# Kernel optimization log

Hardware: AMD Instinct MI355X
Metric: run time of the kernel (lower is better)

The kernel has to match this reference:

```python
import jax, jax.numpy as jnp
import numpy as np

NUM_CLASSES = 10
TAU = 3.3333333


def thermometer_encode(x, thresholds):
    # x: [B, F], thresholds: [F, T] -> binary bits [B, F*T]
    bits = (x[:, :, None] > thresholds[None, :, :]).astype(x.dtype)
    B = x.shape[0]
    return bits.reshape(B, -1)


def lut_layer(h, idx, luts):
    # h: [B, I] activations in [0,1]; idx: [O, n] input mapping; luts: [O, 2^n]
    # Multilinear interpolation over the 2^n LUT corners (gather + fold).
    xs = h[:, idx]                       # [B, O, n] gathered inputs
    B, O, n = xs.shape
    acc = jnp.broadcast_to(luts[None, :, :], (B, O, luts.shape[1]))  # [B, O, 2^n]
    for k in range(n):                   # fold one input bit per step (MSB first)
        half = acc.shape[-1] // 2
        xk = xs[:, :, k:k + 1]           # [B, O, 1]
        acc = acc[..., :half] * (1.0 - xk) + acc[..., half:] * xk
    return acc[..., 0]                   # [B, O]


def group_sum(h, k, tau):
    # h: [B, W] -> [B, k] popcount-style grouped sum scaled by 1/tau
    B, W = h.shape
    return h.reshape(B, k, W // k).sum(axis=-1) / tau


def setup_inputs() -> dict:
    key = jax.random.key(0)
    ks = jax.random.split(key, 6)
    B, F, T = 512, 1024, 3
    I = F * T                            # 3072 thermometer bits
    O1, O2, n = 2000, 1000, 6
    x = jax.random.normal(ks[0], (B, F), dtype=jnp.float32)
    thresholds = jax.random.normal(ks[1], (F, T), dtype=jnp.float32)
    luts1 = jax.random.uniform(ks[2], (O1, 2 ** n), dtype=jnp.float32)
    idx1 = jax.random.randint(ks[3], (O1, n), 0, I, dtype=jnp.int32)
    luts2 = jax.random.uniform(ks[4], (O2, 2 ** n), dtype=jnp.float32)
    idx2 = jax.random.randint(ks[5], (O2, n), 0, O1, dtype=jnp.int32)
    return {"x": x, "thresholds": thresholds, "luts1": luts1, "idx1": idx1,
            "luts2": luts2, "idx2": idx2}


def reference(x, thresholds, luts1, idx1, luts2, idx2):
    h = thermometer_encode(x, thresholds)     # [B, 3072] binary
    h = lut_layer(h, idx1, luts1)             # [B, 2000]
    h = lut_layer(h, idx2, luts2)             # [B, 1000]
    return group_sum(h, NUM_CLASSES, TAU)     # [B, 10]
```

## Files before the change

### kernel.cpp

```cpp
#include <hip/hip_runtime.h>


#define BATCH 512
#define FEAT  1024
#define NBITS (FEAT * 3)
#define O1    2000
#define O2    1000
#define NCLS  10
#define G     2
#define NT    512

__global__ __launch_bounds__(NT) void dwn_fused2(
    const float* __restrict__ x,
    const float* __restrict__ thr,
    const float* __restrict__ luts1,
    const int*   __restrict__ idx1,
    const float* __restrict__ luts2,
    const int*   __restrict__ idx2,
    float* __restrict__ out)
{
    __shared__ unsigned char s_bits[G][NBITS];
    __shared__ float s_h1[G][O1];
    __shared__ float s_h2[G][O2];
    __shared__ float s_part[G * NCLS * 10];

    const int b0 = blockIdx.x * G;
    const int t  = threadIdx.x;

    for (int i = t; i < G * FEAT; i += NT) {
        int r = i >> 10;
        int f = i & (FEAT - 1);
        float xv = x[(b0 + r) * FEAT + f];
        const float* tp = thr + f * 3;
        s_bits[r][f * 3 + 0] = (unsigned char)(xv > tp[0]);
        s_bits[r][f * 3 + 1] = (unsigned char)(xv > tp[1]);
        s_bits[r][f * 3 + 2] = (unsigned char)(xv > tp[2]);
    }
    __syncthreads();

    for (int i = t; i < G * O1; i += NT) {
        int o = i >> 1;
        int r = i & 1;
        const int2* ip = (const int2*)(idx1 + o * 6);
        int2 p0 = ip[0], p1 = ip[1], p2 = ip[2];
        int code = ((int)s_bits[r][p0.x] << 5) | ((int)s_bits[r][p0.y] << 4)
                 | ((int)s_bits[r][p1.x] << 3) | ((int)s_bits[r][p1.y] << 2)
                 | ((int)s_bits[r][p2.x] << 1) |  (int)s_bits[r][p2.y];
        s_h1[r][o] = luts1[o * 64 + code];
    }
    __syncthreads();

    for (int i = t; i < G * O2; i += NT) {
        int o = i >> 1;
        int r = i & 1;
        const int2* ip = (const int2*)(idx2 + o * 6);
        int2 p0 = ip[0], p1 = ip[1], p2 = ip[2];
        float xv0 = s_h1[r][p0.x];
        float xv1 = s_h1[r][p0.y];
        float xv2 = s_h1[r][p1.x];
        float xv3 = s_h1[r][p1.y];
        float xv4 = s_h1[r][p2.x];
        float xv5 = s_h1[r][p2.y];

        const float4* lp = (const float4*)(luts2 + (size_t)o * 64);
        float v[16];
#pragma unroll
        for (int q = 0; q < 16; ++q) {
            float4 e = lp[q];
            float u0 = e.x + xv5 * (e.y - e.x);
            float u1 = e.z + xv5 * (e.w - e.z);
            v[q] = u0 + xv4 * (u1 - u0);
        }
#pragma unroll
        for (int q = 0; q < 8; ++q) v[q] = v[2*q] + xv3 * (v[2*q+1] - v[2*q]);
#pragma unroll
        for (int q = 0; q < 4; ++q) v[q] = v[2*q] + xv2 * (v[2*q+1] - v[2*q]);
#pragma unroll
        for (int q = 0; q < 2; ++q) v[q] = v[2*q] + xv1 * (v[2*q+1] - v[2*q]);
        s_h2[r][o] = v[0] + xv0 * (v[1] - v[0]);
    }
    __syncthreads();

    if (t < G * NCLS * 10) {
        int g = t / 10;
        int p = t % 10;
        int r   = g / NCLS;
        int cls = g % NCLS;
        const float* hp = &s_h2[r][cls * 100 + p * 10];
        float s = 0.0f;
#pragma unroll
        for (int j = 0; j < 10; ++j) s += hp[j];
        s_part[t] = s;
    }
    __syncthreads();
    if (t < G * NCLS) {
        float s = 0.0f;
#pragma unroll
        for (int j = 0; j < 10; ++j) s += s_part[t * 10 + j];
        int r   = t / NCLS;
        int cls = t % NCLS;
        out[(b0 + r) * NCLS + cls] = s / 3.3333333f;
    }
}

extern "C" void kernel_launch(void* const* d_in, const int* in_sizes, int n_in,
                              void* d_out, int out_size, void* d_ws, size_t ws_size,
                              hipStream_t stream) {
    const float* x      = (const float*)d_in[0];
    const float* thr    = (const float*)d_in[1];
    const float* luts1  = (const float*)d_in[2];
    const int*   idx1   = (const int*)  d_in[3];
    const float* luts2  = (const float*)d_in[4];
    const int*   idx2   = (const int*)  d_in[5];
    float* out = (float*)d_out;

    dwn_fused2<<<BATCH / G, NT, 0, stream>>>(x, thr, luts1, idx1, luts2, idx2, out);
}
```

Measured before the change: 79.32 us.

## Split fused kernel into four batch-transposed kernels with ballot-packed bitmasks

Replaces the single fused kernel, which ran 256 blocks of 2 batch rows each, with four kernels. They pack the thermometer bits into wave-ballot 64-bit masks, compute layer 1 and layer 2 with one block per output neuron and one thread per batch row, then reduce the classes. Intermediates live transposed in workspace memory so accesses along the batch are coalesced, and each block's LUT row and index entry are shared by all threads. The cost is global-memory round trips for h1/h2 (about 4 MB plus 2 MB) and three extra kernel launches in exchange for far more parallelism.

Result: slower. 82.33 us (+3.8%).

```diff
diff --git a/kernel.cpp b/kernel.cpp
--- a/kernel.cpp
+++ b/kernel.cpp
@@ -1,118 +1,141 @@
 #include <hip/hip_runtime.h>
 
 
-#define BATCH 512
 #define FEAT  1024
-#define NBITS (FEAT * 3)
 #define O1    2000
 #define O2    1000
 #define NCLS  10
-#define G     2
-#define NT    512
 
-__global__ __launch_bounds__(NT) void dwn_fused2(
+#define WS_BITS_OFF  0
+#define WS_H1_OFF    (256 << 10)
+#define WS_H2_OFF    ((256 << 10) + (4 << 20))
+
+__global__ __launch_bounds__(512) void k1_thermo_pack(
     const float* __restrict__ x,
     const float* __restrict__ thr,
+    unsigned long long* __restrict__ bitsT)
+{
+    const int r    = threadIdx.x;
+    const int w    = r >> 6;
+    const int lane = r & 63;
+    const int f0   = blockIdx.x * 4;
+
+    float4 xv4 = *(const float4*)(x + (size_t)r * FEAT + f0);
+    float xa[4] = {xv4.x, xv4.y, xv4.z, xv4.w};
+
+#pragma unroll
+    for (int f = 0; f < 4; ++f) {
+        const float* tp = thr + (size_t)(f0 + f) * 3;
+#pragma unroll
+        for (int j = 0; j < 3; ++j) {
+            unsigned long long m = __ballot(xa[f] > tp[j]);
+            if (lane == 0)
+                bitsT[(size_t)((f0 + f) * 3 + j) * 8 + w] = m;
+        }
+    }
+}
+
+__global__ __launch_bounds__(512) void k2_layer1(
+    const int*   __restrict__ idx1,
     const float* __restrict__ luts1,
-    const int*   __restrict__ idx1,
+    const unsigned long long* __restrict__ bitsT,
+    float* __restrict__ h1T)
+{
+    const int o    = blockIdx.x;
+    const int r    = threadIdx.x;
+    const int w    = r >> 6;
+    const int lane = r & 63;
+    const int* ip  = idx1 + o * 6;
+
+    unsigned long long m0 = bitsT[(size_t)ip[0] * 8 + w];
+    unsigned long long m1 = bitsT[(size_t)ip[1] * 8 + w];
+    unsigned long long m2 = bitsT[(size_t)ip[2] * 8 + w];
+    unsigned long long m3 = bitsT[(size_t)ip[3] * 8 + w];
+    unsigned long long m4 = bitsT[(size_t)ip[4] * 8 + w];
+    unsigned long long m5 = bitsT[(size_t)ip[5] * 8 + w];
+
+    int code = ((int)((m0 >> lane) & 1ull) << 5)
+             | ((int)((m1 >> lane) & 1ull) << 4)
+             | ((int)((m2 >> lane) & 1ull) << 3)
+             | ((int)((m3 >> lane) & 1ull) << 2)
+             | ((int)((m4 >> lane) & 1ull) << 1)
+             |  (int)((m5 >> lane) & 1ull);
+
+    h1T[(size_t)o * 512 + r] = luts1[o * 64 + code];
+}
+
+__global__ __launch_bounds__(512) void k3_layer2(
+    const int*   __restrict__ idx2,
     const float* __restrict__ luts2,
-    const int*   __restrict__ idx2,
+    const float* __restrict__ h1T,
+    float* __restrict__ h2T)
+{
+    const int o   = blockIdx.x;
+    const int r   = threadIdx.x;
+    const int* ip = idx2 + o * 6;
+
+    float xv0 = h1T[(size_t)ip[0] * 512 + r];
+    float xv1 = h1T[(size_t)ip[1] * 512 + r];
+    float xv2 = h1T[(size_t)ip[2] * 512 + r];
+    float xv3 = h1T[(size_t)ip[3] * 512 + r];
+    float xv4 = h1T[(size_t)ip[4] * 512 + r];
+    float xv5 = h1T[(size_t)ip[5] * 512 + r];
+
+    const float4* lp = (const float4*)(luts2 + (size_t)o * 64);
+    float v[16];
+#pragma unroll
+    for (int q = 0; q < 16; ++q) {
+        float4 e = lp[q];
+        float u0 = e.x + xv5 * (e.y - e.x);
+        float u1 = e.z + xv5 * (e.w - e.z);
+        v[q] = u0 + xv4 * (u1 - u0);
+    }
+#pragma unroll
+    for (int q = 0; q < 8; ++q) v[q] = v[2*q] + xv3 * (v[2*q+1] - v[2*q]);
+#pragma unroll
+    for (int q = 0; q < 4; ++q) v[q] = v[2*q] + xv2 * (v[2*q+1] - v[2*q]);
+#pragma unroll
+    for (int q = 0; q < 2; ++q) v[q] = v[2*q] + xv1 * (v[2*q+1] - v[2*q]);
+    h2T[(size_t)o * 512 + r] = v[0] + xv0 * (v[1] - v[0]);
+}
+
+__global__ __launch_bounds__(256) void k4_reduce(
+    const float* __restrict__ h2T,
     float* __restrict__ out)
 {
-    __shared__ unsigned char s_bits[G][NBITS];
-    __shared__ float s_h1[G][O1];
-    __shared__ float s_h2[G][O2];
-    __shared__ float s_part[G * NCLS * 10];
+    const int c = blockIdx.x >> 1;
+    const int r = ((blockIdx.x & 1) << 8) | threadIdx.x;
+    const float* hp = h2T + (size_t)c * 100 * 512 + r;
 
-    const int b0 = blockIdx.x * G;
-    const int t  = threadIdx.x;
-
-    for (int i = t; i < G * FEAT; i += NT) {
-        int r = i >> 10;
-        int f = i & (FEAT - 1);
-        float xv = x[(b0 + r) * FEAT + f];
-        const float* tp = thr + f * 3;
-        s_bits[r][f * 3 + 0] = (unsigned char)(xv > tp[0]);
-        s_bits[r][f * 3 + 1] = (unsigned char)(xv > tp[1]);
-        s_bits[r][f * 3 + 2] = (unsigned char)(xv > tp[2]);
+    float s = 0.0f;
+#pragma unroll
+    for (int p = 0; p < 10; ++p) {
+        float s2 = 0.0f;
+#pragma unroll
+        for (int j = 0; j < 10; ++j) s2 += hp[(size_t)(p * 10 + j) * 512];
+        s += s2;
     }
-    __syncthreads();
-
-    for (int i = t; i < G * O1; i += NT) {
-        int o = i >> 1;
-        int r = i & 1;
-        const int2* ip = (const int2*)(idx1 + o * 6);
-        int2 p0 = ip[0], p1 = ip[1], p2 = ip[2];
-        int code = ((int)s_bits[r][p0.x] << 5) | ((int)s_bits[r][p0.y] << 4)
-                 | ((int)s_bits[r][p1.x] << 3) | ((int)s_bits[r][p1.y] << 2)
-                 | ((int)s_bits[r][p2.x] << 1) |  (int)s_bits[r][p2.y];
-        s_h1[r][o] = luts1[o * 64 + code];
-    }
-    __syncthreads();
-
-    for (int i = t; i < G * O2; i += NT) {
-        int o = i >> 1;
-        int r = i & 1;
-        const int2* ip = (const int2*)(idx2 + o * 6);
-        int2 p0 = ip[0], p1 = ip[1], p2 = ip[2];
-        float xv0 = s_h1[r][p0.x];
-        float xv1 = s_h1[r][p0.y];
-        float xv2 = s_h1[r][p1.x];
-        float xv3 = s_h1[r][p1.y];
-        float xv4 = s_h1[r][p2.x];
-        float xv5 = s_h1[r][p2.y];
-
-        const float4* lp = (const float4*)(luts2 + (size_t)o * 64);
-        float v[16];
-#pragma unroll
-        for (int q = 0; q < 16; ++q) {
-            float4 e = lp[q];
-            float u0 = e.x + xv5 * (e.y - e.x);
-            float u1 = e.z + xv5 * (e.w - e.z);
-            v[q] = u0 + xv4 * (u1 - u0);
-        }
-#pragma unroll
-        for (int q = 0; q < 8; ++q) v[q] = v[2*q] + xv3 * (v[2*q+1] - v[2*q]);
-#pragma unroll
-        for (int q = 0; q < 4; ++q) v[q] = v[2*q] + xv2 * (v[2*q+1] - v[2*q]);
-#pragma unroll
-        for (int q = 0; q < 2; ++q) v[q] = v[2*q] + xv1 * (v[2*q+1] - v[2*q]);
-        s_h2[r][o] = v[0] + xv0 * (v[1] - v[0]);
-    }
-    __syncthreads();
-
-    if (t < G * NCLS * 10) {
-        int g = t / 10;
-        int p = t % 10;
-        int r   = g / NCLS;
-        int cls = g % NCLS;
-        const float* hp = &s_h2[r][cls * 100 + p * 10];
-        float s = 0.0f;
-#pragma unroll
-        for (int j = 0; j < 10; ++j) s += hp[j];
-        s_part[t] = s;
-    }
-    __syncthreads();
-    if (t < G * NCLS) {
-        float s = 0.0f;
-#pragma unroll
-        for (int j = 0; j < 10; ++j) s += s_part[t * 10 + j];
-        int r   = t / NCLS;
-        int cls = t % NCLS;
-        out[(b0 + r) * NCLS + cls] = s / 3.3333333f;
-    }
+    out[r * NCLS + c] = s / 3.3333333f;
 }
 
 extern "C" void kernel_launch(void* const* d_in, const int* in_sizes, int n_in,
                               void* d_out, int out_size, void* d_ws, size_t ws_size,
                               hipStream_t stream) {
-    const float* x      = (const float*)d_in[0];
-    const float* thr    = (const float*)d_in[1];
-    const float* luts1  = (const float*)d_in[2];
-    const int*   idx1   = (const int*)  d_in[3];
-    const float* luts2  = (const float*)d_in[4];
-    const int*   idx2   = (const int*)  d_in[5];
+    const float* x     = (const float*)d_in[0];
+    const float* thr   = (const float*)d_in[1];
+    const float* luts1 = (const float*)d_in[2];
+    const int*   idx1  = (const int*)  d_in[3];
+    const float* luts2 = (const float*)d_in[4];
+    const int*   idx2  = (const int*)  d_in[5];
     float* out = (float*)d_out;
 
-    dwn_fused2<<<BATCH / G, NT, 0, stream>>>(x, thr, luts1, idx1, luts2, idx2, out);
+    char* ws = (char*)d_ws;
+    unsigned long long* bitsT = (unsigned long long*)(ws + WS_BITS_OFF);
+    float* h1T = (float*)(ws + WS_H1_OFF);
+    float* h2T = (float*)(ws + WS_H2_OFF);
+
+    k1_thermo_pack<<<FEAT / 4, 512, 0, stream>>>(x, thr, bitsT);
+    k2_layer1<<<O1, 512, 0, stream>>>(idx1, luts1, bitsT, h1T);
+    k3_layer2<<<O2, 512, 0, stream>>>(idx2, luts2, h1T, h2T);
+    k4_reduce<<<NCLS * 2, 256, 0, stream>>>(h2T, out);
 }
```

## Pack thermometer bits via wave ballot and double block size

Applied to the files above, without the earlier changes.

Thermometer encoding now uses a wavefront ballot to build 32-bit bitmasks in shared memory, replacing the byte-per-bit layout. This shrinks the shared footprint and makes the first-layer code lookups bit extractions. Block size goes from 512 to 1024 threads with launch bounds requesting 4 blocks per CU, and the strided loops are unrolled with bounds checks. The larger blocks and the min-blocks hint may limit registers in the second-layer interpolation, which needs 16 floats plus the gathered inputs.

Measured after the change: 78.56 us. Within noise of the previous version (-1.0%).

```diff
diff --git a/kernel.cpp b/kernel.cpp
--- a/kernel.cpp
+++ b/kernel.cpp
@@ -8,9 +8,10 @@
 #define O2    1000
 #define NCLS  10
 #define G     2
-#define NT    512
+#define NB    (BATCH / G)
+#define NT    1024
 
-__global__ __launch_bounds__(NT) void dwn_fused2(
+__global__ __launch_bounds__(NT, 4) void dwn_fused(
     const float* __restrict__ x,
     const float* __restrict__ thr,
     const float* __restrict__ luts1,
@@ -19,65 +20,85 @@
     const int*   __restrict__ idx2,
     float* __restrict__ out)
 {
-    __shared__ unsigned char s_bits[G][NBITS];
+    __shared__ unsigned s_bw[G][NBITS / 32];
     __shared__ float s_h1[G][O1];
     __shared__ float s_h2[G][O2];
     __shared__ float s_part[G * NCLS * 10];
 
-    const int b0 = blockIdx.x * G;
-    const int t  = threadIdx.x;
+    const int t    = threadIdx.x;
+    const int lane = t & 63;
+    const int wl   = t >> 6;
+    const int b0   = blockIdx.x * G;
 
-    for (int i = t; i < G * FEAT; i += NT) {
-        int r = i >> 10;
-        int f = i & (FEAT - 1);
-        float xv = x[(b0 + r) * FEAT + f];
-        const float* tp = thr + f * 3;
-        s_bits[r][f * 3 + 0] = (unsigned char)(xv > tp[0]);
-        s_bits[r][f * 3 + 1] = (unsigned char)(xv > tp[1]);
-        s_bits[r][f * 3 + 2] = (unsigned char)(xv > tp[2]);
+#pragma unroll
+    for (int k = 0; k < 6; ++k) {
+        const int task = k * 16 + wl;
+        const int r  = task & 1;
+        const int g  = task >> 1;
+        const int bi = (g << 6) | lane;
+        const int f  = bi / 3;
+        const float xv = x[(b0 + r) * FEAT + f];
+        const float tv = thr[bi];
+        const unsigned long long m = __ballot(xv > tv);
+        if (lane == 0) {
+            s_bw[r][2 * g]     = (unsigned)m;
+            s_bw[r][2 * g + 1] = (unsigned)(m >> 32);
+        }
     }
     __syncthreads();
 
-    for (int i = t; i < G * O1; i += NT) {
-        int o = i >> 1;
-        int r = i & 1;
-        const int2* ip = (const int2*)(idx1 + o * 6);
-        int2 p0 = ip[0], p1 = ip[1], p2 = ip[2];
-        int code = ((int)s_bits[r][p0.x] << 5) | ((int)s_bits[r][p0.y] << 4)
-                 | ((int)s_bits[r][p1.x] << 3) | ((int)s_bits[r][p1.y] << 2)
-                 | ((int)s_bits[r][p2.x] << 1) |  (int)s_bits[r][p2.y];
-        s_h1[r][o] = luts1[o * 64 + code];
+#pragma unroll
+    for (int k = 0; k < 4; ++k) {
+        const int i = t + k * NT;
+        if (i < G * O1) {
+            const int o = i >> 1;
+            const int r = i & 1;
+            const int2* ip = (const int2*)(idx1 + o * 6);
+            const int2 p0 = ip[0], p1 = ip[1], p2 = ip[2];
+            const int code =
+                  ((int)((s_bw[r][p0.x >> 5] >> (p0.x & 31)) & 1u) << 5)
+                | ((int)((s_bw[r][p0.y >> 5] >> (p0.y & 31)) & 1u) << 4)
+                | ((int)((s_bw[r][p1.x >> 5] >> (p1.x & 31)) & 1u) << 3)
+                | ((int)((s_bw[r][p1.y >> 5] >> (p1.y & 31)) & 1u) << 2)
+                | ((int)((s_bw[r][p2.x >> 5] >> (p2.x & 31)) & 1u) << 1)
+                |  (int)((s_bw[r][p2.y >> 5] >> (p2.y & 31)) & 1u);
+            s_h1[r][o] = luts1[o * 64 + code];
+        }
     }
     __syncthreads();
 
-    for (int i = t; i < G * O2; i += NT) {
-        int o = i >> 1;
-        int r = i & 1;
-        const int2* ip = (const int2*)(idx2 + o * 6);
-        int2 p0 = ip[0], p1 = ip[1], p2 = ip[2];
-        float xv0 = s_h1[r][p0.x];
-        float xv1 = s_h1[r][p0.y];
-        float xv2 = s_h1[r][p1.x];
-        float xv3 = s_h1[r][p1.y];
-        float xv4 = s_h1[r][p2.x];
-        float xv5 = s_h1[r][p2.y];
+#pragma unroll
+    for (int k = 0; k < 2; ++k) {
+        const int i = t + k * NT;
+        if (i < G * O2) {
+            const int o = i >> 1;
+            const int r = i & 1;
+            const int2* ip = (const int2*)(idx2 + o * 6);
+            const int2 p0 = ip[0], p1 = ip[1], p2 = ip[2];
+            const float xv0 = s_h1[r][p0.x];
+            const float xv1 = s_h1[r][p0.y];
+            const float xv2 = s_h1[r][p1.x];
+            const float xv3 = s_h1[r][p1.y];
+            const float xv4 = s_h1[r][p2.x];
+            const float xv5 = s_h1[r][p2.y];
 
-        const float4* lp = (const float4*)(luts2 + (size_t)o * 64);
-        float v[16];
+            const float4* lp = (const float4*)(luts2 + (size_t)o * 64);
+            float v[16];
 #pragma unroll
-        for (int q = 0; q < 16; ++q) {
-            float4 e = lp[q];
-            float u0 = e.x + xv5 * (e.y - e.x);
-            float u1 = e.z + xv5 * (e.w - e.z);
-            v[q] = u0 + xv4 * (u1 - u0);
+            for (int q = 0; q < 16; ++q) {
+                float4 e = lp[q];
+                float u0 = e.x + xv5 * (e.y - e.x);
+                float u1 = e.z + xv5 * (e.w - e.z);
+                v[q] = u0 + xv4 * (u1 - u0);
+            }
+#pragma unroll
+            for (int q = 0; q < 8; ++q) v[q] = v[2*q] + xv3 * (v[2*q+1] - v[2*q]);
+#pragma unroll
+            for (int q = 0; q < 4; ++q) v[q] = v[2*q] + xv2 * (v[2*q+1] - v[2*q]);
+#pragma unroll
+            for (int q = 0; q < 2; ++q) v[q] = v[2*q] + xv1 * (v[2*q+1] - v[2*q]);
+            s_h2[r][o] = v[0] + xv0 * (v[1] - v[0]);
         }
-#pragma unroll
-        for (int q = 0; q < 8; ++q) v[q] = v[2*q] + xv3 * (v[2*q+1] - v[2*q]);
-#pragma unroll
-        for (int q = 0; q < 4; ++q) v[q] = v[2*q] + xv2 * (v[2*q+1] - v[2*q]);
-#pragma unroll
-        for (int q = 0; q < 2; ++q) v[q] = v[2*q] + xv1 * (v[2*q+1] - v[2*q]);
-        s_h2[r][o] = v[0] + xv0 * (v[1] - v[0]);
     }
     __syncthreads();
 
@@ -106,13 +127,13 @@
 extern "C" void kernel_launch(void* const* d_in, const int* in_sizes, int n_in,
                               void* d_out, int out_size, void* d_ws, size_t ws_size,
                               hipStream_t stream) {
-    const float* x      = (const float*)d_in[0];
-    const float* thr    = (const float*)d_in[1];
-    const float* luts1  = (const float*)d_in[2];
-    const int*   idx1   = (const int*)  d_in[3];
-    const float* luts2  = (const float*)d_in[4];
-    const int*   idx2   = (const int*)  d_in[5];
+    const float* x     = (const float*)d_in[0];
+    const float* thr   = (const float*)d_in[1];
+    const float* luts1 = (const float*)d_in[2];
+    const int*   idx1  = (const int*)  d_in[3];
+    const float* luts2 = (const float*)d_in[4];
+    const int*   idx2  = (const int*)  d_in[5];
     float* out = (float*)d_out;
 
-    dwn_fused2<<<BATCH / G, NT, 0, stream>>>(x, thr, luts1, idx1, luts2, idx2, out);
+    dwn_fused<<<NB, NT, 0, stream>>>(x, thr, luts1, idx1, luts2, idx2, out);
 }
```
